# Performance work log

Measured on AMD Instinct MI355X. Metric: run time of the kernel, lower is better.

Reference implementation:

```python
import jax, jax.numpy as jnp
import numpy as np

N = 16384          # number of vectors to quantize (flattened leading dims)
K = 2 ** 14        # codebook_size = 2**bits_per_codeword
D = 64             # vector_dim


def setup_inputs() -> dict:
    key = jax.random.key(0)
    k1, k2, k3, k4 = jax.random.split(key, 4)
    x_re = jax.random.normal(k1, (N, D), dtype=jnp.float32)
    x_im = jax.random.normal(k2, (N, D), dtype=jnp.float32)
    # random complex codebook, normalized so each row has unit complex L2 norm
    cb_re = jax.random.normal(k3, (K, D), dtype=jnp.float32)
    cb_im = jax.random.normal(k4, (K, D), dtype=jnp.float32)
    norm = jnp.sqrt(jnp.sum(cb_re * cb_re + cb_im * cb_im, axis=1, keepdims=True))
    cb_re = cb_re / norm
    cb_im = cb_im / norm
    return {"x_re": x_re, "x_im": x_im, "cb_re": cb_re, "cb_im": cb_im}


def reference(x_re, x_im, cb_re, cb_im):
    # complex inner product conj(x) . c, expanded in real arithmetic:
    #   Re = x_re.c_re + x_im.c_im ;  Im = x_re.c_im - x_im.c_re
    dot_re = jnp.einsum('nd,kd->nk', x_re, cb_re) + jnp.einsum('nd,kd->nk', x_im, cb_im)
    dot_im = jnp.einsum('nd,kd->nk', x_re, cb_im) - jnp.einsum('nd,kd->nk', x_im, cb_re)
    mag = jnp.sqrt(dot_re * dot_re + dot_im * dot_im)  # [N, K] abs of complex dot
    indices = jnp.argmax(mag, axis=-1)                 # [N] int
    # reconstruction: gather codebook rows (call() with int input)
    recon = jnp.stack([cb_re[indices], cb_im[indices]], axis=-1)  # [N, D, 2] (re, im)
    return indices, recon
```

## Files before the change

kernel.cpp:

```cpp
#include <hip/hip_runtime.h>

#define NROWS 16384
#define KCB   16384
#define DD    64
#define BM    256
#define CSPLIT 16
#define COLS_PER_BLOCK 1024
#define TILE_COLS 128
#define NTILES (COLS_PER_BLOCK / TILE_COLS)
#define NCHUNK (TILE_COLS / 16)
#define CAP 2048
#define DELTA 0.45f

typedef __attribute__((ext_vector_type(8))) short bf16x8;
typedef __attribute__((ext_vector_type(4))) float f32x4;

__device__ __forceinline__ unsigned pk_bf16(float lo, float hi) {
    unsigned a = __float_as_uint(lo);
    unsigned b = __float_as_uint(hi);
    a += 0x7FFFu + ((a >> 16) & 1u);
    b += 0x7FFFu + ((b >> 16) & 1u);
    return (a >> 16) | (b & 0xFFFF0000u);
}

__device__ __forceinline__ bf16x8 mk8(unsigned a, unsigned b, unsigned c, unsigned d) {
    union { uint4 u; bf16x8 v; } x;
    x.u = make_uint4(a, b, c, d);
    return x.v;
}

__device__ __forceinline__ unsigned swz(unsigned row, unsigned byte_in_row) {
    return row * 128u + (byte_in_row ^ ((row & 7u) << 4));
}

__global__ __launch_bounds__(256) void prep(
    const float* __restrict__ cb_re, const float* __restrict__ cb_im,
    uint4* __restrict__ cbr_ws, uint4* __restrict__ cbi_ws,
    unsigned* __restrict__ row_max_bits, unsigned long long* __restrict__ best_packed,
    int do_conv)
{
    int id = blockIdx.x * 256 + threadIdx.x;
    if (id < NROWS) { row_max_bits[id] = 0u; best_packed[id] = 0ull; }
    if (!do_conv) return;
    int row = id >> 4;
    int sub = id & 15;
    const float* src = (sub >> 3) ? cb_im : cb_re;
    uint4* dst = (sub >> 3) ? cbi_ws : cbr_ws;
    int d0 = (sub & 7) * 8;
    const float4* p = (const float4*)(src + (size_t)row * DD + d0);
    float4 f0 = p[0], f1 = p[1];
    dst[row * 8 + (sub & 7)] = make_uint4(
        pk_bf16(f0.x, f0.y), pk_bf16(f0.z, f0.w),
        pk_bf16(f1.x, f1.y), pk_bf16(f1.z, f1.w));
}

template<int PASS, bool PRE>
__global__ __launch_bounds__(512, 2) void score_kernel(
    const float* __restrict__ x_re, const float* __restrict__ x_im,
    const float* __restrict__ cb_re, const float* __restrict__ cb_im,
    const uint4* __restrict__ cbr_ws, const uint4* __restrict__ cbi_ws,
    unsigned* __restrict__ row_max_bits,
    unsigned long long* __restrict__ best_packed)
{
    __shared__ char Bls[2][2][TILE_COLS * 128];
    __shared__ unsigned cand[CAP];
    __shared__ int cand_cnt;

    const int tid  = threadIdx.x;
    const int lane = tid & 63;
    const int wid  = tid >> 6;
    const int row0 = blockIdx.x * BM;
    const int col0 = blockIdx.y * COLS_PER_BLOCK;
    const int l15  = lane & 15;
    const int lhi  = lane >> 4;

    if (tid == 0) cand_cnt = 0;

    bf16x8 Ar[2][2], Ai[2][2], Ain[2][2];
#pragma unroll
    for (int a = 0; a < 2; ++a) {
        const int row = row0 + wid * 32 + a * 16 + l15;
#pragma unroll
        for (int ks = 0; ks < 2; ++ks) {
            const float4* pr = (const float4*)(x_re + (size_t)row * DD + ks * 32 + lhi * 8);
            const float4* pi = (const float4*)(x_im + (size_t)row * DD + ks * 32 + lhi * 8);
            float4 r0 = pr[0], r1 = pr[1];
            float4 i0 = pi[0], i1 = pi[1];
            Ar[a][ks] = mk8(pk_bf16(r0.x, r0.y), pk_bf16(r0.z, r0.w),
                            pk_bf16(r1.x, r1.y), pk_bf16(r1.z, r1.w));
            Ai[a][ks] = mk8(pk_bf16(i0.x, i0.y), pk_bf16(i0.z, i0.w),
                            pk_bf16(i1.x, i1.y), pk_bf16(i1.z, i1.w));
            Ain[a][ks] = Ai[a][ks] ^ (short)0x8000;
        }
    }

    float rm[2][4];
    float thr[2][4];
#pragma unroll
    for (int a = 0; a < 2; ++a)
#pragma unroll
        for (int r = 0; r < 4; ++r) rm[a][r] = 0.0f;
    if (PASS == 2) {
#pragma unroll
        for (int a = 0; a < 2; ++a)
#pragma unroll
            for (int r = 0; r < 4; ++r) {
                int n = row0 + wid * 32 + a * 16 + lhi * 4 + r;
                float mx = __uint_as_float(row_max_bits[n]);
                float tm = sqrtf(mx) - DELTA;
                thr[a][r] = (tm > 0.0f) ? tm * tm : -1.0f;
            }
    }

    const int scol  = tid >> 2;
    const int sboff = (tid & 3) * 32;
    uint4 g[4];

    auto stage_load = [&](int t) {
        if (PRE) {
            const size_t base = (size_t)(col0 + t * TILE_COLS) * 8 + tid * 2;
            g[0] = cbr_ws[base];     g[1] = cbr_ws[base + 1];
            g[2] = cbi_ws[base];     g[3] = cbi_ws[base + 1];
        } else {
            const int col = col0 + t * TILE_COLS + scol;
            const int d0  = (tid & 3) * 16;
            const float4* pr = (const float4*)(cb_re + (size_t)col * DD + d0);
            const float4* pi = (const float4*)(cb_im + (size_t)col * DD + d0);
            float4 a0 = pr[0], a1 = pr[1], a2 = pr[2], a3 = pr[3];
            float4 b0 = pi[0], b1 = pi[1], b2 = pi[2], b3 = pi[3];
            g[0] = make_uint4(pk_bf16(a0.x,a0.y), pk_bf16(a0.z,a0.w), pk_bf16(a1.x,a1.y), pk_bf16(a1.z,a1.w));
            g[1] = make_uint4(pk_bf16(a2.x,a2.y), pk_bf16(a2.z,a2.w), pk_bf16(a3.x,a3.y), pk_bf16(a3.z,a3.w));
            g[2] = make_uint4(pk_bf16(b0.x,b0.y), pk_bf16(b0.z,b0.w), pk_bf16(b1.x,b1.y), pk_bf16(b1.z,b1.w));
            g[3] = make_uint4(pk_bf16(b2.x,b2.y), pk_bf16(b2.z,b2.w), pk_bf16(b3.x,b3.y), pk_bf16(b3.z,b3.w));
        }
    };
    auto stage_write = [&](int buf) {
        unsigned o0 = swz(scol, sboff);
        unsigned o1 = swz(scol, sboff + 16);
        *(uint4*)(&Bls[buf][0][0] + o0) = g[0];
        *(uint4*)(&Bls[buf][0][0] + o1) = g[1];
        *(uint4*)(&Bls[buf][1][0] + o0) = g[2];
        *(uint4*)(&Bls[buf][1][0] + o1) = g[3];
    };

    stage_load(0);
    stage_write(0);
    __syncthreads();

    for (int t = 0; t < NTILES; ++t) {
        const int cur = t & 1;
        if (t + 1 < NTILES) stage_load(t + 1);

        const char* B0 = &Bls[cur][0][0];
        const char* B1 = &Bls[cur][1][0];

        for (int ch = 0; ch < NCHUNK; ++ch) {
            const int colLocal = ch * 16 + l15;

            f32x4 accre[2], accim[2];
#pragma unroll
            for (int a = 0; a < 2; ++a) {
                accre[a] = (f32x4){0.f, 0.f, 0.f, 0.f};
                accim[a] = (f32x4){0.f, 0.f, 0.f, 0.f};
            }

#pragma unroll
            for (int ks = 0; ks < 2; ++ks) {
                unsigned off = swz(colLocal, ks * 64 + lhi * 16);
                bf16x8 br = *(const bf16x8*)(B0 + off);
                bf16x8 bi = *(const bf16x8*)(B1 + off);
#pragma unroll
                for (int a = 0; a < 2; ++a)
                    accre[a] = __builtin_amdgcn_mfma_f32_16x16x32_bf16(Ar[a][ks], br, accre[a], 0, 0, 0);
#pragma unroll
                for (int a = 0; a < 2; ++a)
                    accre[a] = __builtin_amdgcn_mfma_f32_16x16x32_bf16(Ai[a][ks], bi, accre[a], 0, 0, 0);
#pragma unroll
                for (int a = 0; a < 2; ++a)
                    accim[a] = __builtin_amdgcn_mfma_f32_16x16x32_bf16(Ar[a][ks], bi, accim[a], 0, 0, 0);
#pragma unroll
                for (int a = 0; a < 2; ++a)
                    accim[a] = __builtin_amdgcn_mfma_f32_16x16x32_bf16(Ain[a][ks], br, accim[a], 0, 0, 0);
            }

#pragma unroll
            for (int a = 0; a < 2; ++a)
#pragma unroll
                for (int r = 0; r < 4; ++r) {
                    float re = accre[a][r], im = accim[a][r];
                    float m2 = fmaf(re, re, im * im);
                    if (PASS == 1) {
                        rm[a][r] = fmaxf(rm[a][r], m2);
                    } else {
                        if (m2 >= thr[a][r]) {
                            int n = row0 + wid * 32 + a * 16 + lhi * 4 + r;
                            int k = col0 + t * TILE_COLS + ch * 16 + l15;
                            int idx = atomicAdd(&cand_cnt, 1);
                            if (idx < CAP) cand[idx] = ((unsigned)n << 14) | (unsigned)k;
                        }
                    }
                }
        }

        if (t + 1 < NTILES) {
            stage_write(1 - cur);
            __syncthreads();
        }
    }
    __syncthreads();

    if (PASS == 1) {
#pragma unroll
        for (int m = 1; m < 16; m <<= 1)
#pragma unroll
            for (int a = 0; a < 2; ++a)
#pragma unroll
                for (int r = 0; r < 4; ++r)
                    rm[a][r] = fmaxf(rm[a][r], __shfl_xor(rm[a][r], m, 64));
        if (l15 == 0) {
#pragma unroll
            for (int a = 0; a < 2; ++a)
#pragma unroll
                for (int r = 0; r < 4; ++r) {
                    int n = row0 + wid * 32 + a * 16 + lhi * 4 + r;
                    atomicMax(&row_max_bits[n], __float_as_uint(rm[a][r]));
                }
        }
    } else {
        int cnt = cand_cnt < CAP ? cand_cnt : CAP;
        for (int i = tid; i < cnt; i += 512) {
            unsigned e = cand[i];
            int n = (int)(e >> 14);
            int k = (int)(e & 16383u);
            const float* xr = x_re + (size_t)n * DD;
            const float* xi = x_im + (size_t)n * DD;
            const float* cr = cb_re + (size_t)k * DD;
            const float* ci = cb_im + (size_t)k * DD;
            float accr = 0.0f, acci = 0.0f;
            for (int d = 0; d < DD; ++d) {
                float xrv = xr[d], xiv = xi[d], crv = cr[d], civ = ci[d];
                accr = fmaf(xrv, crv, accr);
                accr = fmaf(xiv, civ, accr);
                acci = fmaf(xrv, civ, acci);
                acci = fmaf(-xiv, crv, acci);
            }
            float m2 = accr * accr + acci * acci;
            unsigned long long key =
                ((unsigned long long)__float_as_uint(m2) << 32) | (unsigned)(~(unsigned)k);
            atomicMax(&best_packed[n], key);
        }
    }
}

__global__ __launch_bounds__(256) void finalize(
    const unsigned long long* __restrict__ best_packed,
    const float* __restrict__ cb_re, const float* __restrict__ cb_im,
    float* __restrict__ out)
{
    const int wave = threadIdx.x >> 6;
    const int lane = threadIdx.x & 63;
    const int n = blockIdx.x * 4 + wave;
    if (n >= NROWS) return;

    unsigned long long p = best_packed[n];
    unsigned k = ~(unsigned)(p & 0xFFFFFFFFull);

    if (lane == 0) out[n] = (float)k;

    float re = cb_re[(size_t)k * DD + lane];
    float im = cb_im[(size_t)k * DD + lane];
    float2* ro = reinterpret_cast<float2*>(out + NROWS);
    ro[(size_t)n * DD + lane] = make_float2(re, im);
}

extern "C" void kernel_launch(void* const* d_in, const int* in_sizes, int n_in,
                              void* d_out, int out_size, void* d_ws, size_t ws_size,
                              hipStream_t stream)
{
    const float* x_re  = (const float*)d_in[0];
    const float* x_im  = (const float*)d_in[1];
    const float* cb_re = (const float*)d_in[2];
    const float* cb_im = (const float*)d_in[3];
    float* out = (float*)d_out;

    const size_t CB_BYTES = (size_t)KCB * DD * 2;
    const size_t NEED = 2 * CB_BYTES + NROWS * 4 + NROWS * 8;
    const bool pre = (ws_size >= NEED);

    uint4* cbr_ws; uint4* cbi_ws; unsigned* row_max_bits; unsigned long long* best_packed;
    if (pre) {
        cbr_ws = (uint4*)d_ws;
        cbi_ws = (uint4*)((char*)d_ws + CB_BYTES);
        row_max_bits = (unsigned*)((char*)d_ws + 2 * CB_BYTES);
        best_packed  = (unsigned long long*)((char*)d_ws + 2 * CB_BYTES + NROWS * 4);
    } else {
        cbr_ws = (uint4*)d_ws; cbi_ws = (uint4*)d_ws;
        row_max_bits = (unsigned*)d_ws;
        best_packed  = (unsigned long long*)((char*)d_ws + NROWS * 4);
    }

    prep<<<pre ? 1024 : (NROWS / 256), 256, 0, stream>>>(
        cb_re, cb_im, cbr_ws, cbi_ws, row_max_bits, best_packed, pre ? 1 : 0);

    dim3 grid(NROWS / BM, CSPLIT);
    if (pre) {
        score_kernel<1, true><<<grid, 512, 0, stream>>>(x_re, x_im, cb_re, cb_im,
            cbr_ws, cbi_ws, row_max_bits, best_packed);
        score_kernel<2, true><<<grid, 512, 0, stream>>>(x_re, x_im, cb_re, cb_im,
            cbr_ws, cbi_ws, row_max_bits, best_packed);
    } else {
        score_kernel<1, false><<<grid, 512, 0, stream>>>(x_re, x_im, cb_re, cb_im,
            cbr_ws, cbi_ws, row_max_bits, best_packed);
        score_kernel<2, false><<<grid, 512, 0, stream>>>(x_re, x_im, cb_re, cb_im,
            cbr_ws, cbi_ws, row_max_bits, best_packed);
    }

    finalize<<<NROWS / 4, 256, 0, stream>>>(best_packed, cb_re, cb_im, out);
}
```

Baseline: 310.6 us.

## Pre-swizzle bf16 codebook tiles and stream them directly into LDS

```diff
diff --git a/kernel.cpp b/kernel.cpp
--- a/kernel.cpp
+++ b/kernel.cpp
@@ -11,6 +11,7 @@
 #define NCHUNK (TILE_COLS / 16)
 #define CAP 2048
 #define DELTA 0.45f
+#define TILE_BYTES 32768
 
 typedef __attribute__((ext_vector_type(8))) short bf16x8;
 typedef __attribute__((ext_vector_type(4))) float f32x4;
@@ -33,32 +34,40 @@
     return row * 128u + (byte_in_row ^ ((row & 7u) << 4));
 }
 
+__device__ __forceinline__ void gload_lds16(const void* g, void* l) {
+    __builtin_amdgcn_global_load_lds(
+        (__attribute__((address_space(1))) void*)(g),
+        (__attribute__((address_space(3))) void*)(l), 16, 0, 0);
+}
+
 __global__ __launch_bounds__(256) void prep(
     const float* __restrict__ cb_re, const float* __restrict__ cb_im,
-    uint4* __restrict__ cbr_ws, uint4* __restrict__ cbi_ws,
+    uint4* __restrict__ cb_sw,
     unsigned* __restrict__ row_max_bits, unsigned long long* __restrict__ best_packed,
     int do_conv)
 {
     int id = blockIdx.x * 256 + threadIdx.x;
     if (id < NROWS) { row_max_bits[id] = 0u; best_packed[id] = 0ull; }
     if (!do_conv) return;
-    int row = id >> 4;
-    int sub = id & 15;
-    const float* src = (sub >> 3) ? cb_im : cb_re;
-    uint4* dst = (sub >> 3) ? cbi_ws : cbr_ws;
-    int d0 = (sub & 7) * 8;
-    const float4* p = (const float4*)(src + (size_t)row * DD + d0);
+    int u   = id & 1023;
+    int arr = (id >> 10) & 1;
+    int gt  = id >> 11;
+    int c   = u >> 3;
+    int b   = ((u & 7) * 16) ^ ((c & 7) << 4);
+    int col = gt * TILE_COLS + c;
+    int d0  = b >> 1;
+    const float* src = arr ? cb_im : cb_re;
+    const float4* p = (const float4*)(src + (size_t)col * DD + d0);
     float4 f0 = p[0], f1 = p[1];
-    dst[row * 8 + (sub & 7)] = make_uint4(
-        pk_bf16(f0.x, f0.y), pk_bf16(f0.z, f0.w),
-        pk_bf16(f1.x, f1.y), pk_bf16(f1.z, f1.w));
+    cb_sw[id] = make_uint4(pk_bf16(f0.x, f0.y), pk_bf16(f0.z, f0.w),
+                           pk_bf16(f1.x, f1.y), pk_bf16(f1.z, f1.w));
 }
 
 template<int PASS, bool PRE>
 __global__ __launch_bounds__(512, 2) void score_kernel(
     const float* __restrict__ x_re, const float* __restrict__ x_im,
     const float* __restrict__ cb_re, const float* __restrict__ cb_im,
-    const uint4* __restrict__ cbr_ws, const uint4* __restrict__ cbi_ws,
+    const char* __restrict__ cb_sw,
     unsigned* __restrict__ row_max_bits,
     unsigned long long* __restrict__ best_packed)
 {
@@ -76,21 +85,29 @@
 
     if (tid == 0) cand_cnt = 0;
 
-    bf16x8 Ar[2][2], Ai[2][2], Ain[2][2];
+    bf16x8 Ar[2][2], Ai[2][2];
 #pragma unroll
     for (int a = 0; a < 2; ++a) {
         const int row = row0 + wid * 32 + a * 16 + l15;
-#pragma unroll
-        for (int ks = 0; ks < 2; ++ks) {
-            const float4* pr = (const float4*)(x_re + (size_t)row * DD + ks * 32 + lhi * 8);
-            const float4* pi = (const float4*)(x_im + (size_t)row * DD + ks * 32 + lhi * 8);
+        {
+            const float4* pr = (const float4*)(x_re + (size_t)row * DD + lhi * 8);
+            const float4* pi = (const float4*)(x_im + (size_t)row * DD + lhi * 8);
             float4 r0 = pr[0], r1 = pr[1];
             float4 i0 = pi[0], i1 = pi[1];
-            Ar[a][ks] = mk8(pk_bf16(r0.x, r0.y), pk_bf16(r0.z, r0.w),
-                            pk_bf16(r1.x, r1.y), pk_bf16(r1.z, r1.w));
-            Ai[a][ks] = mk8(pk_bf16(i0.x, i0.y), pk_bf16(i0.z, i0.w),
-                            pk_bf16(i1.x, i1.y), pk_bf16(i1.z, i1.w));
-            Ain[a][ks] = Ai[a][ks] ^ (short)0x8000;
+            Ar[a][0] = mk8(pk_bf16(r0.x, r0.y), pk_bf16(r0.z, r0.w),
+                           pk_bf16(r1.x, r1.y), pk_bf16(r1.z, r1.w));
+            Ai[a][0] = mk8(pk_bf16(i0.x, i0.y), pk_bf16(i0.z, i0.w),
+                           pk_bf16(i1.x, i1.y), pk_bf16(i1.z, i1.w));
+        }
+        {
+            const float4* pr = (const float4*)(x_re + (size_t)row * DD + 32 + lhi * 8);
+            const float4* pi = (const float4*)(x_im + (size_t)row * DD + 32 + lhi * 8);
+            float4 r0 = pr[0], r1 = pr[1];
+            float4 i0 = pi[0], i1 = pi[1];
+            Ar[a][1] = mk8(pk_bf16(r0.x, r0.y), pk_bf16(r0.z, r0.w),
+                           pk_bf16(r1.x, r1.y), pk_bf16(r1.z, r1.w));
+            Ai[a][1] = mk8(pk_bf16(i0.x, i0.y), pk_bf16(i0.z, i0.w),
+                           pk_bf16(i1.x, i1.y), pk_bf16(i1.z, i1.w));
         }
     }
 
@@ -112,16 +129,95 @@
             }
     }
 
-    const int scol  = tid >> 2;
-    const int sboff = (tid & 3) * 32;
-    uint4 g[4];
-
-    auto stage_load = [&](int t) {
-        if (PRE) {
-            const size_t base = (size_t)(col0 + t * TILE_COLS) * 8 + tid * 2;
-            g[0] = cbr_ws[base];     g[1] = cbr_ws[base + 1];
-            g[2] = cbi_ws[base];     g[3] = cbi_ws[base + 1];
-        } else {
+#define CHUNK_BODY(T_IDX, CH)                                                   \
+    {                                                                           \
+        const char* B0 = &Bls[(T_IDX) & 1][0][0];                               \
+        const char* B1 = &Bls[(T_IDX) & 1][1][0];                               \
+        const int colLocal = (CH) * 16 + l15;                                   \
+        unsigned off0 = swz(colLocal, lhi * 16);                                \
+        unsigned off1 = swz(colLocal, 64 + lhi * 16);                           \
+        bf16x8 br0 = *(const bf16x8*)(B0 + off0);                               \
+        bf16x8 bi0 = *(const bf16x8*)(B1 + off0);                               \
+        bf16x8 br1 = *(const bf16x8*)(B0 + off1);                               \
+        bf16x8 bi1 = *(const bf16x8*)(B1 + off1);                               \
+        f32x4 accre[2], accim[2];                                               \
+        _Pragma("unroll")                                                       \
+        for (int a = 0; a < 2; ++a) {                                           \
+            accre[a] = (f32x4){0.f, 0.f, 0.f, 0.f};                             \
+            accim[a] = (f32x4){0.f, 0.f, 0.f, 0.f};                             \
+        }                                                                       \
+        _Pragma("unroll")                                                       \
+        for (int a = 0; a < 2; ++a) {                                           \
+            accre[a] = __builtin_amdgcn_mfma_f32_16x16x32_bf16(Ar[a][0], br0, accre[a], 0, 0, 0); \
+            accre[a] = __builtin_amdgcn_mfma_f32_16x16x32_bf16(Ai[a][0], bi0, accre[a], 0, 0, 0); \
+            accre[a] = __builtin_amdgcn_mfma_f32_16x16x32_bf16(Ar[a][1], br1, accre[a], 0, 0, 0); \
+            accre[a] = __builtin_amdgcn_mfma_f32_16x16x32_bf16(Ai[a][1], bi1, accre[a], 0, 0, 0); \
+            accim[a] = __builtin_amdgcn_mfma_f32_16x16x32_bf16(Ar[a][0], bi0, accim[a], 0, 0, 0); \
+            accim[a] = __builtin_amdgcn_mfma_f32_16x16x32_bf16(Ar[a][1], bi1, accim[a], 0, 0, 0); \
+        }                                                                       \
+        br0 = br0 ^ (short)0x8000;                                              \
+        br1 = br1 ^ (short)0x8000;                                              \
+        _Pragma("unroll")                                                       \
+        for (int a = 0; a < 2; ++a) {                                           \
+            accim[a] = __builtin_amdgcn_mfma_f32_16x16x32_bf16(Ai[a][0], br0, accim[a], 0, 0, 0); \
+            accim[a] = __builtin_amdgcn_mfma_f32_16x16x32_bf16(Ai[a][1], br1, accim[a], 0, 0, 0); \
+        }                                                                       \
+        _Pragma("unroll")                                                       \
+        for (int a = 0; a < 2; ++a)                                             \
+            _Pragma("unroll")                                                   \
+            for (int r = 0; r < 4; ++r) {                                       \
+                float re = accre[a][r], im = accim[a][r];                       \
+                float m2 = fmaf(re, re, im * im);                               \
+                if (PASS == 1) {                                                \
+                    rm[a][r] = fmaxf(rm[a][r], m2);                             \
+                } else {                                                        \
+                    if (m2 >= thr[a][r]) {                                      \
+                        int n = row0 + wid * 32 + a * 16 + lhi * 4 + r;         \
+                        int k = col0 + (T_IDX) * TILE_COLS + (CH) * 16 + l15;   \
+                        int idx = atomicAdd(&cand_cnt, 1);                      \
+                        if (idx < CAP) cand[idx] = ((unsigned)n << 14) | (unsigned)k; \
+                    }                                                           \
+                }                                                               \
+            }                                                                   \
+    }
+
+    if constexpr (PRE) {
+        const char* tile_base = cb_sw + (size_t)blockIdx.y * NTILES * TILE_BYTES;
+        auto stage = [&](int buf, int t) {
+            const char* src = tile_base + (size_t)t * TILE_BYTES;
+            char* dst = &Bls[buf][0][0];
+#pragma unroll
+            for (int j = 0; j < 4; ++j)
+                gload_lds16(src + j * 8192 + tid * 16, dst + j * 8192 + tid * 16);
+        };
+
+        stage(0, 0);
+        __syncthreads();
+
+        for (int t = 0; t < NTILES; ++t) {
+            const int cur = t & 1;
+            if (t + 1 < NTILES) {
+                stage(cur ^ 1, t + 1);
+                asm volatile("s_waitcnt vmcnt(4)" ::: "memory");
+            } else {
+                asm volatile("s_waitcnt vmcnt(0)" ::: "memory");
+            }
+            __builtin_amdgcn_sched_barrier(0);
+            __builtin_amdgcn_s_barrier();
+            __builtin_amdgcn_sched_barrier(0);
+
+            for (int ch = 0; ch < NCHUNK; ++ch)
+                CHUNK_BODY(t, ch)
+
+            __builtin_amdgcn_sched_barrier(0);
+            __builtin_amdgcn_s_barrier();
+        }
+        __syncthreads();
+    } else {
+        const int scol  = tid >> 2;
+        const int sboff = (tid & 3) * 32;
+        uint4 g[4];
+        auto stage_load = [&](int t) {
             const int col = col0 + t * TILE_COLS + scol;
             const int d0  = (tid & 3) * 16;
             const float4* pr = (const float4*)(cb_re + (size_t)col * DD + d0);
@@ -132,82 +228,30 @@
             g[1] = make_uint4(pk_bf16(a2.x,a2.y), pk_bf16(a2.z,a2.w), pk_bf16(a3.x,a3.y), pk_bf16(a3.z,a3.w));
             g[2] = make_uint4(pk_bf16(b0.x,b0.y), pk_bf16(b0.z,b0.w), pk_bf16(b1.x,b1.y), pk_bf16(b1.z,b1.w));
             g[3] = make_uint4(pk_bf16(b2.x,b2.y), pk_bf16(b2.z,b2.w), pk_bf16(b3.x,b3.y), pk_bf16(b3.z,b3.w));
-        }
-    };
-    auto stage_write = [&](int buf) {
-        unsigned o0 = swz(scol, sboff);
-        unsigned o1 = swz(scol, sboff + 16);
-        *(uint4*)(&Bls[buf][0][0] + o0) = g[0];
-        *(uint4*)(&Bls[buf][0][0] + o1) = g[1];
-        *(uint4*)(&Bls[buf][1][0] + o0) = g[2];
-        *(uint4*)(&Bls[buf][1][0] + o1) = g[3];
-    };
-
-    stage_load(0);
-    stage_write(0);
-    __syncthreads();
-
-    for (int t = 0; t < NTILES; ++t) {
-        const int cur = t & 1;
-        if (t + 1 < NTILES) stage_load(t + 1);
-
-        const char* B0 = &Bls[cur][0][0];
-        const char* B1 = &Bls[cur][1][0];
-
-        for (int ch = 0; ch < NCHUNK; ++ch) {
-            const int colLocal = ch * 16 + l15;
-
-            f32x4 accre[2], accim[2];
-#pragma unroll
-            for (int a = 0; a < 2; ++a) {
-                accre[a] = (f32x4){0.f, 0.f, 0.f, 0.f};
-                accim[a] = (f32x4){0.f, 0.f, 0.f, 0.f};
+        };
+        auto stage_write = [&](int buf) {
+            unsigned o0 = swz(scol, sboff);
+            unsigned o1 = swz(scol, sboff + 16);
+            *(uint4*)(&Bls[buf][0][0] + o0) = g[0];
+            *(uint4*)(&Bls[buf][0][0] + o1) = g[1];
+            *(uint4*)(&Bls[buf][1][0] + o0) = g[2];
+            *(uint4*)(&Bls[buf][1][0] + o1) = g[3];
+        };
+        stage_load(0);
+        stage_write(0);
+        __syncthreads();
+        for (int t = 0; t < NTILES; ++t) {
+            if (t + 1 < NTILES) stage_load(t + 1);
+            for (int ch = 0; ch < NCHUNK; ++ch)
+                CHUNK_BODY(t, ch)
+            if (t + 1 < NTILES) {
+                stage_write(1 - (t & 1));
+                __syncthreads();
             }
-
-#pragma unroll
-            for (int ks = 0; ks < 2; ++ks) {
-                unsigned off = swz(colLocal, ks * 64 + lhi * 16);
-                bf16x8 br = *(const bf16x8*)(B0 + off);
-                bf16x8 bi = *(const bf16x8*)(B1 + off);
-#pragma unroll
-                for (int a = 0; a < 2; ++a)
-                    accre[a] = __builtin_amdgcn_mfma_f32_16x16x32_bf16(Ar[a][ks], br, accre[a], 0, 0, 0);
-#pragma unroll
-                for (int a = 0; a < 2; ++a)
-                    accre[a] = __builtin_amdgcn_mfma_f32_16x16x32_bf16(Ai[a][ks], bi, accre[a], 0, 0, 0);
-#pragma unroll
-                for (int a = 0; a < 2; ++a)
-                    accim[a] = __builtin_amdgcn_mfma_f32_16x16x32_bf16(Ar[a][ks], bi, accim[a], 0, 0, 0);
-#pragma unroll
-                for (int a = 0; a < 2; ++a)
-                    accim[a] = __builtin_amdgcn_mfma_f32_16x16x32_bf16(Ain[a][ks], br, accim[a], 0, 0, 0);
-            }
-
-#pragma unroll
-            for (int a = 0; a < 2; ++a)
-#pragma unroll
-                for (int r = 0; r < 4; ++r) {
-                    float re = accre[a][r], im = accim[a][r];
-                    float m2 = fmaf(re, re, im * im);
-                    if (PASS == 1) {
-                        rm[a][r] = fmaxf(rm[a][r], m2);
-                    } else {
-                        if (m2 >= thr[a][r]) {
-                            int n = row0 + wid * 32 + a * 16 + lhi * 4 + r;
-                            int k = col0 + t * TILE_COLS + ch * 16 + l15;
-                            int idx = atomicAdd(&cand_cnt, 1);
-                            if (idx < CAP) cand[idx] = ((unsigned)n << 14) | (unsigned)k;
-                        }
-                    }
-                }
-        }
-
-        if (t + 1 < NTILES) {
-            stage_write(1 - cur);
-            __syncthreads();
-        }
-    }
-    __syncthreads();
+        }
+        __syncthreads();
+    }
+#undef CHUNK_BODY
 
     if (PASS == 1) {
 #pragma unroll
@@ -283,36 +327,35 @@
     const float* cb_im = (const float*)d_in[3];
     float* out = (float*)d_out;
 
-    const size_t CB_BYTES = (size_t)KCB * DD * 2;
-    const size_t NEED = 2 * CB_BYTES + NROWS * 4 + NROWS * 8;
+    const size_t CB_SW_BYTES = (size_t)(KCB / TILE_COLS) * TILE_BYTES;
+    const size_t NEED = CB_SW_BYTES + NROWS * 4 + NROWS * 8;
     const bool pre = (ws_size >= NEED);
 
-    uint4* cbr_ws; uint4* cbi_ws; unsigned* row_max_bits; unsigned long long* best_packed;
+    const char* cb_sw = (const char*)d_ws;
+    unsigned* row_max_bits;
+    unsigned long long* best_packed;
     if (pre) {
-        cbr_ws = (uint4*)d_ws;
-        cbi_ws = (uint4*)((char*)d_ws + CB_BYTES);
-        row_max_bits = (unsigned*)((char*)d_ws + 2 * CB_BYTES);
-        best_packed  = (unsigned long long*)((char*)d_ws + 2 * CB_BYTES + NROWS * 4);
+        row_max_bits = (unsigned*)((char*)d_ws + CB_SW_BYTES);
+        best_packed  = (unsigned long long*)((char*)d_ws + CB_SW_BYTES + NROWS * 4);
     } else {
-        cbr_ws = (uint4*)d_ws; cbi_ws = (uint4*)d_ws;
         row_max_bits = (unsigned*)d_ws;
         best_packed  = (unsigned long long*)((char*)d_ws + NROWS * 4);
     }
 
     prep<<<pre ? 1024 : (NROWS / 256), 256, 0, stream>>>(
-        cb_re, cb_im, cbr_ws, cbi_ws, row_max_bits, best_packed, pre ? 1 : 0);
+        cb_re, cb_im, (uint4*)d_ws, row_max_bits, best_packed, pre ? 1 : 0);
 
     dim3 grid(NROWS / BM, CSPLIT);
     if (pre) {
         score_kernel<1, true><<<grid, 512, 0, stream>>>(x_re, x_im, cb_re, cb_im,
-            cbr_ws, cbi_ws, row_max_bits, best_packed);
+            cb_sw, row_max_bits, best_packed);
         score_kernel<2, true><<<grid, 512, 0, stream>>>(x_re, x_im, cb_re, cb_im,
-            cbr_ws, cbi_ws, row_max_bits, best_packed);
+            cb_sw, row_max_bits, best_packed);
     } else {
         score_kernel<1, false><<<grid, 512, 0, stream>>>(x_re, x_im, cb_re, cb_im,
-            cbr_ws, cbi_ws, row_max_bits, best_packed);
+            cb_sw, row_max_bits, best_packed);
         score_kernel<2, false><<<grid, 512, 0, stream>>>(x_re, x_im, cb_re, cb_im,
-            cbr_ws, cbi_ws, row_max_bits, best_packed);
+            cb_sw, row_max_bits, best_packed);
     }
 
     finalize<<<NROWS / 4, 256, 0, stream>>>(best_packed, cb_re, cb_im, out);
```

Result: faster. 268.7 us (-13.5%).
